# Kernel tuning notes

Measured on AMD Instinct MI355X. Metric: run time of the kernel, lower is better.

## Reference

```python
import jax, jax.numpy as jnp
import numpy as np

EPS = 1e-6


def setup_inputs() -> dict:
    key = jax.random.key(0)
    k1, k2, k3, k4 = jax.random.split(key, 4)
    dim = 3072
    seq = 8192
    x = jax.random.normal(k1, (1, seq, dim), dtype=jnp.float32)
    emb = jax.random.normal(k2, (1, dim), dtype=jnp.float32)
    W = jax.random.normal(k3, (3 * dim, dim), dtype=jnp.float32) * 0.02
    b = jax.random.normal(k4, (3 * dim,), dtype=jnp.float32) * 0.02
    return {"x": x, "emb": emb, "W": W, "b": b}


def reference(x, emb, W, b):
    # SiLU + linear (dequantized-equivalent of int4 AWQ GEMV): [1,dim]x[dim,3dim] -> [1,3dim]
    e = jnp.dot(jax.nn.silu(emb), W.T) + b
    # Interleaved unpack: reshape (1, dim, 3) then unbind last axis (matches torch code)
    e3 = e.reshape(1, -1, 3)
    shift_msa = e3[..., 0]  # [1, dim]
    scale_msa = e3[..., 1]
    gate_msa = e3[..., 2]
    # LayerNorm over last dim, no affine, eps=1e-6
    mean = jnp.mean(x, axis=-1, keepdims=True)
    var = jnp.mean(jnp.square(x - mean), axis=-1, keepdims=True)
    xn = (x - mean) * jax.lax.rsqrt(var + EPS)
    out = xn * scale_msa[:, None] + shift_msa[:, None]
    return (out, gate_msa)
```

## Files before the change

kernel.cpp:

```cpp
#include <hip/hip_runtime.h>
#include <math.h>

#define DIM 3072
#define SEQ 8192

__device__ __forceinline__ float silu_f(float v) {
    return v / (1.0f + __expf(-v));
}

__global__ __launch_bounds__(256) void gemv3_kernel(
    const float* __restrict__ emb, const float* __restrict__ W,
    const float* __restrict__ b, float* __restrict__ shift,
    float* __restrict__ scale, float* __restrict__ gate)
{
    __shared__ float s[DIM];
    __shared__ float red[3][4];
    const int t = threadIdx.x;
    const float4* emb4 = (const float4*)emb;
    float4* s4 = (float4*)s;

    #pragma unroll
    for (int k = 0; k < 3; ++k) {
        int i = t + k * 256;
        float4 v = emb4[i];
        v.x = silu_f(v.x); v.y = silu_f(v.y);
        v.z = silu_f(v.z); v.w = silu_f(v.w);
        s4[i] = v;
    }
    __syncthreads();

    const int i0 = blockIdx.x;
    float acc[3] = {0.f, 0.f, 0.f};
    #pragma unroll
    for (int r = 0; r < 3; ++r) {
        const float4* w4 = (const float4*)(W + (size_t)(3 * i0 + r) * DIM);
        #pragma unroll
        for (int k = 0; k < 3; ++k) {
            int i = t + k * 256;
            float4 w = w4[i];
            float4 v = s4[i];
            acc[r] += w.x * v.x + w.y * v.y + w.z * v.z + w.w * v.w;
        }
    }

    #pragma unroll
    for (int off = 32; off > 0; off >>= 1) {
        #pragma unroll
        for (int r = 0; r < 3; ++r) acc[r] += __shfl_down(acc[r], off, 64);
    }
    const int wave = t >> 6;
    if ((t & 63) == 0) {
        #pragma unroll
        for (int r = 0; r < 3; ++r) red[r][wave] = acc[r];
    }
    __syncthreads();
    if (t == 0) {
        float v0 = red[0][0] + red[0][1] + red[0][2] + red[0][3] + b[3 * i0 + 0];
        float v1 = red[1][0] + red[1][1] + red[1][2] + red[1][3] + b[3 * i0 + 1];
        float v2 = red[2][0] + red[2][1] + red[2][2] + red[2][3] + b[3 * i0 + 2];
        shift[i0] = v0;
        scale[i0] = v1;
        gate[i0]  = v2;
    }
}

__global__ __launch_bounds__(256) void ln_affine_kernel(
    const float* __restrict__ x, const float* __restrict__ shift,
    const float* __restrict__ scale, float* __restrict__ out)
{
    const int row = blockIdx.x;
    const int t = threadIdx.x;
    const float4* x4 = (const float4*)(x + (size_t)row * DIM);
    float4* o4 = (float4*)(out + (size_t)row * DIM);
    const float4* sc4 = (const float4*)scale;
    const float4* sh4 = (const float4*)shift;

    float4 v[3];
    float sum = 0.f, sq = 0.f;
    #pragma unroll
    for (int k = 0; k < 3; ++k) {
        v[k] = x4[t + k * 256];
        sum += v[k].x + v[k].y + v[k].z + v[k].w;
        sq  += v[k].x * v[k].x + v[k].y * v[k].y + v[k].z * v[k].z + v[k].w * v[k].w;
    }

    #pragma unroll
    for (int off = 32; off > 0; off >>= 1) {
        sum += __shfl_down(sum, off, 64);
        sq  += __shfl_down(sq,  off, 64);
    }
    __shared__ float rsum[4], rsq[4];
    __shared__ float mean_s, rstd_s;
    const int wave = t >> 6;
    if ((t & 63) == 0) { rsum[wave] = sum; rsq[wave] = sq; }
    __syncthreads();
    if (t == 0) {
        float S = rsum[0] + rsum[1] + rsum[2] + rsum[3];
        float Q = rsq[0] + rsq[1] + rsq[2] + rsq[3];
        float mean = S * (1.0f / DIM);
        float var = Q * (1.0f / DIM) - mean * mean;
        mean_s = mean;
        rstd_s = rsqrtf(var + 1e-6f);
    }
    __syncthreads();
    const float mean = mean_s, rstd = rstd_s;

    #pragma unroll
    for (int k = 0; k < 3; ++k) {
        int i = t + k * 256;
        float4 sc = sc4[i];
        float4 sh = sh4[i];
        float4 r;
        r.x = (v[k].x - mean) * rstd * sc.x + sh.x;
        r.y = (v[k].y - mean) * rstd * sc.y + sh.y;
        r.z = (v[k].z - mean) * rstd * sc.z + sh.z;
        r.w = (v[k].w - mean) * rstd * sc.w + sh.w;
        o4[i] = r;
    }
}

extern "C" void kernel_launch(void* const* d_in, const int* in_sizes, int n_in,
                              void* d_out, int out_size, void* d_ws, size_t ws_size,
                              hipStream_t stream) {
    const float* x   = (const float*)d_in[0];
    const float* emb = (const float*)d_in[1];
    const float* W   = (const float*)d_in[2];
    const float* b   = (const float*)d_in[3];
    float* out  = (float*)d_out;
    float* gate = out + (size_t)SEQ * DIM;
    float* shift = (float*)d_ws;
    float* scale = shift + DIM;

    gemv3_kernel<<<DIM, 256, 0, stream>>>(emb, W, b, shift, scale, gate);
    ln_affine_kernel<<<SEQ, 256, 0, stream>>>(x, shift, scale, out);
}
```

Measured before the change: 65.13 us.

## Map one wavefront per row in GEMV and LayerNorm kernels

Both kernels now assign a single 64-lane wavefront to each row, so 4 rows go to each 256-thread block. The block-level shared-memory reductions and __syncthreads are replaced by wave-only xor shuffles. This removes the cross-wave sync overhead in LayerNorm and lets the GEMV write each output row straight from one wave. In exchange each thread holds 12 float4 values in registers, which raises register pressure, and the silu staging into shared memory now runs once per 4 rows instead of once per output triple.

```diff
diff --git a/kernel.cpp b/kernel.cpp
--- a/kernel.cpp
+++ b/kernel.cpp
@@ -3,18 +3,18 @@
 
 #define DIM 3072
 #define SEQ 8192
+#define NROWS (3 * DIM)
 
 __device__ __forceinline__ float silu_f(float v) {
     return v / (1.0f + __expf(-v));
 }
 
-__global__ __launch_bounds__(256) void gemv3_kernel(
+__global__ __launch_bounds__(256, 4) void gemv3_kernel(
     const float* __restrict__ emb, const float* __restrict__ W,
     const float* __restrict__ b, float* __restrict__ shift,
     float* __restrict__ scale, float* __restrict__ gate)
 {
     __shared__ float s[DIM];
-    __shared__ float red[3][4];
     const int t = threadIdx.x;
     const float4* emb4 = (const float4*)emb;
     float4* s4 = (float4*)s;
@@ -29,85 +29,68 @@
     }
     __syncthreads();
 
-    const int i0 = blockIdx.x;
-    float acc[3] = {0.f, 0.f, 0.f};
+    const int wid = t >> 6;
+    const int lane = t & 63;
+    const int row = blockIdx.x * 4 + wid;
+    const float4* w4 = (const float4*)(W + (size_t)row * DIM);
+
+    float acc = 0.f;
     #pragma unroll
-    for (int r = 0; r < 3; ++r) {
-        const float4* w4 = (const float4*)(W + (size_t)(3 * i0 + r) * DIM);
-        #pragma unroll
-        for (int k = 0; k < 3; ++k) {
-            int i = t + k * 256;
-            float4 w = w4[i];
-            float4 v = s4[i];
-            acc[r] += w.x * v.x + w.y * v.y + w.z * v.z + w.w * v.w;
-        }
+    for (int k = 0; k < 12; ++k) {
+        int i = lane + 64 * k;
+        float4 w = w4[i];
+        float4 v = s4[i];
+        acc += w.x * v.x + w.y * v.y + w.z * v.z + w.w * v.w;
     }
 
     #pragma unroll
-    for (int off = 32; off > 0; off >>= 1) {
-        #pragma unroll
-        for (int r = 0; r < 3; ++r) acc[r] += __shfl_down(acc[r], off, 64);
-    }
-    const int wave = t >> 6;
-    if ((t & 63) == 0) {
-        #pragma unroll
-        for (int r = 0; r < 3; ++r) red[r][wave] = acc[r];
-    }
-    __syncthreads();
-    if (t == 0) {
-        float v0 = red[0][0] + red[0][1] + red[0][2] + red[0][3] + b[3 * i0 + 0];
-        float v1 = red[1][0] + red[1][1] + red[1][2] + red[1][3] + b[3 * i0 + 1];
-        float v2 = red[2][0] + red[2][1] + red[2][2] + red[2][3] + b[3 * i0 + 2];
-        shift[i0] = v0;
-        scale[i0] = v1;
-        gate[i0]  = v2;
+    for (int off = 32; off > 0; off >>= 1)
+        acc += __shfl_xor(acc, off, 64);
+
+    if (lane == 0) {
+        float e = acc + b[row];
+        int i = row / 3;
+        int r = row - 3 * i;
+        if (r == 0)      shift[i] = e;
+        else if (r == 1) scale[i] = e;
+        else             gate[i]  = e;
     }
 }
 
-__global__ __launch_bounds__(256) void ln_affine_kernel(
+__global__ __launch_bounds__(256, 4) void ln_affine_kernel(
     const float* __restrict__ x, const float* __restrict__ shift,
     const float* __restrict__ scale, float* __restrict__ out)
 {
-    const int row = blockIdx.x;
     const int t = threadIdx.x;
+    const int wid = t >> 6;
+    const int lane = t & 63;
+    const int row = blockIdx.x * 4 + wid;
     const float4* x4 = (const float4*)(x + (size_t)row * DIM);
     float4* o4 = (float4*)(out + (size_t)row * DIM);
     const float4* sc4 = (const float4*)scale;
     const float4* sh4 = (const float4*)shift;
 
-    float4 v[3];
+    float4 v[12];
     float sum = 0.f, sq = 0.f;
     #pragma unroll
-    for (int k = 0; k < 3; ++k) {
-        v[k] = x4[t + k * 256];
+    for (int k = 0; k < 12; ++k) {
+        v[k] = x4[lane + 64 * k];
         sum += v[k].x + v[k].y + v[k].z + v[k].w;
         sq  += v[k].x * v[k].x + v[k].y * v[k].y + v[k].z * v[k].z + v[k].w * v[k].w;
     }
 
     #pragma unroll
     for (int off = 32; off > 0; off >>= 1) {
-        sum += __shfl_down(sum, off, 64);
-        sq  += __shfl_down(sq,  off, 64);
+        sum += __shfl_xor(sum, off, 64);
+        sq  += __shfl_xor(sq,  off, 64);
     }
-    __shared__ float rsum[4], rsq[4];
-    __shared__ float mean_s, rstd_s;
-    const int wave = t >> 6;
-    if ((t & 63) == 0) { rsum[wave] = sum; rsq[wave] = sq; }
-    __syncthreads();
-    if (t == 0) {
-        float S = rsum[0] + rsum[1] + rsum[2] + rsum[3];
-        float Q = rsq[0] + rsq[1] + rsq[2] + rsq[3];
-        float mean = S * (1.0f / DIM);
-        float var = Q * (1.0f / DIM) - mean * mean;
-        mean_s = mean;
-        rstd_s = rsqrtf(var + 1e-6f);
-    }
-    __syncthreads();
-    const float mean = mean_s, rstd = rstd_s;
 
-    #pragma unroll
-    for (int k = 0; k < 3; ++k) {
-        int i = t + k * 256;
+    const float mean = sum * (1.0f / DIM);
+    const float rstd = rsqrtf(sq * (1.0f / DIM) - mean * mean + 1e-6f);
+
+    #pragma unroll 4
+    for (int k = 0; k < 12; ++k) {
+        int i = lane + 64 * k;
         float4 sc = sc4[i];
         float4 sh = sh4[i];
         float4 r;
@@ -131,6 +114,6 @@
     float* shift = (float*)d_ws;
     float* scale = shift + DIM;
 
-    gemv3_kernel<<<DIM, 256, 0, stream>>>(emb, W, b, shift, scale, gate);
-    ln_affine_kernel<<<SEQ, 256, 0, stream>>>(x, shift, scale, out);
+    gemv3_kernel<<<NROWS / 4, 256, 0, stream>>>(emb, W, b, shift, scale, gate);
+    ln_affine_kernel<<<SEQ / 4, 256, 0, stream>>>(x, shift, scale, out);
 }
```

Result: slower. 118.2 us (+81.5%).
